# Performance work log

Hardware: AMD Instinct MI355X
Metric: run time of the kernel (lower is better)

The kernel has to match this reference:

```python
import jax, jax.numpy as jnp
import numpy as np

DIM = 256
N_SLOTS = 4096
HEADS = 4
RANK = 32
TOPK = 32
BATCH = 4
LN_EPS = 1e-5


def _layer_norm(x, gamma, beta):
    m = jnp.mean(x, axis=-1, keepdims=True)
    v = jnp.var(x, axis=-1, keepdims=True)
    return (x - m) * jax.lax.rsqrt(v + LN_EPS) * gamma + beta


def _unit_normalize(v):
    n = jnp.sqrt(jnp.sum(v * v, axis=-1, keepdims=True))
    return v / jnp.maximum(n, 1e-6)


def _signed_softmax(x, axis):
    # sign(x) * softmax(|x|): 'signed_abs_softmax' compression
    return jnp.sign(x) * jax.nn.softmax(jnp.abs(x), axis=axis)


def setup_inputs() -> dict:
    key = jax.random.key(0)
    k1, k2, k3, k4 = jax.random.split(key, 4)
    return {
        "batch_size": BATCH,
        "init_state": 0.02 * jax.random.normal(k1, (N_SLOTS,), dtype=jnp.float32),
        "init_val": 0.02 * jax.random.normal(k2, (N_SLOTS, DIM), dtype=jnp.float32),
        "ln_gamma": jnp.ones((DIM,), dtype=jnp.float32),
        "ln_beta": jnp.zeros((DIM,), dtype=jnp.float32),
        "Wq": jax.random.normal(k3, (HEADS, DIM, RANK), dtype=jnp.float32) / np.sqrt(DIM),
        "Wk": jax.random.normal(k4, (HEADS, DIM, RANK), dtype=jnp.float32) / np.sqrt(DIM),
    }


def reference(batch_size, init_state, init_val, ln_gamma, ln_beta, Wq, Wk):
    B = int(batch_size)
    # ---- initialize(): LayerNorm + unit-normalize values, signed-softmax state ----
    val0 = _unit_normalize(_layer_norm(init_val, ln_gamma, ln_beta))  # [N, D]
    val = jnp.broadcast_to(val0[None], (B, N_SLOTS, DIM))             # [B, N, D]
    state = _signed_softmax(jnp.broadcast_to(init_state[None], (B, N_SLOTS)), axis=-1)

    # ---- SparsePropagation: low-rank multi-head pairwise scores ----
    q = jnp.einsum("bnd,hdr->bhnr", val, Wq)  # [B, H, N, R]
    k = jnp.einsum("bnd,hdr->bhnr", val, Wk)  # [B, H, N, R]
    scores = jnp.einsum("bhnr,bhmr->bnm", q, k)  # [B, N, N] (summed over heads)

    # top-k edges per node by |score| (signed routing)
    _, idx = jax.lax.top_k(jnp.abs(scores), TOPK)            # idx: [B, N, K]
    s = jnp.take_along_axis(scores, idx, axis=-1)            # signed scores [B, N, K]
    w = _signed_softmax(s, axis=-1)                          # edge weights [B, N, K]

    # gather neighbor values and aggregate messages
    vj = jnp.take_along_axis(val[:, None, :, :].repeat(1, axis=1),
                             idx[..., None].repeat(DIM, axis=-1),
                             axis=2) if False else val[jnp.arange(B)[:, None, None], idx]  # [B, N, K, D]
    msg = jnp.einsum("bnk,bnkd->bnd", w, vj)                 # [B, N, D]

    # residual + direction-only (unit-normalized) values
    out_val = _unit_normalize(val + msg)
    return out_val
```

## Files before the change

### kernel.cpp

```cpp
#include <hip/hip_runtime.h>
#include <hip/hip_bf16.h>
#include <math.h>

#define N_SLOTS 4096
#define DIM 256
#define HEADS 4
#define RANK 32
#define TOPK 32
#define QK 128

typedef __attribute__((ext_vector_type(8))) short short8;
typedef __attribute__((ext_vector_type(4))) float f32x4;

__device__ __forceinline__ float block_sum256(float v, float* red) {
#pragma unroll
  for (int o = 32; o > 0; o >>= 1) v += __shfl_xor(v, o);
  int lane = threadIdx.x & 63, wid = threadIdx.x >> 6;
  if (lane == 0) red[wid] = v;
  __syncthreads();
  v = red[0] + red[1] + red[2] + red[3];
  __syncthreads();
  return v;
}

__global__ __launch_bounds__(256) void ln_unit_kernel(
    const float* __restrict__ x, const float* __restrict__ g,
    const float* __restrict__ b, float* __restrict__ val0) {
  __shared__ float red[4];
  int n = blockIdx.x, t = threadIdx.x;
  float v = x[n * DIM + t];
  float mean = block_sum256(v, red) * (1.0f / DIM);
  float d = v - mean;
  float var = block_sum256(d * d, red) * (1.0f / DIM);
  float y = d * rsqrtf(var + 1e-5f) * g[t] + b[t];
  float ss = block_sum256(y * y, red);
  y = y / fmaxf(sqrtf(ss), 1e-6f);
  val0[n * DIM + t] = y;
}

#define QR 4
__global__ __launch_bounds__(256) void qk2_kernel(
    const float* __restrict__ val0, const float* __restrict__ Wq,
    const float* __restrict__ Wk, __hip_bfloat16* __restrict__ qh,
    __hip_bfloat16* __restrict__ ql, __hip_bfloat16* __restrict__ kh,
    __hip_bfloat16* __restrict__ kl) {
  __shared__ float vrow[QR][DIM];
  int t = threadIdx.x;
  int n0 = blockIdx.x * QR;
#pragma unroll
  for (int j = 0; j < QR; ++j) {
    int idx = j * 256 + t;
    vrow[idx >> 8][idx & 255] = val0[(size_t)n0 * DIM + idx];
  }
  __syncthreads();
  int half = t >> 7, u = t & 127, h = u >> 5, r = u & 31;
  const float* wp = (half ? Wk : Wq) + (size_t)h * DIM * RANK + r;
  float acc[QR];
#pragma unroll
  for (int i = 0; i < QR; ++i) acc[i] = 0.f;
#pragma unroll 8
  for (int d = 0; d < DIM; ++d) {
    float w = wp[d * RANK];
#pragma unroll
    for (int i = 0; i < QR; ++i) acc[i] = fmaf(vrow[i][d], w, acc[i]);
  }
  __hip_bfloat16* oh = half ? kh : qh;
  __hip_bfloat16* ol = half ? kl : ql;
#pragma unroll
  for (int i = 0; i < QR; ++i) {
    size_t o = (size_t)(n0 + i) * QK + u;
    __hip_bfloat16 hi = __float2bfloat16(acc[i]);
    oh[o] = hi;
    ol[o] = __float2bfloat16(acc[i] - __bfloat162float(hi));
  }
}

#define TPAD 68
__device__ __forceinline__ int swz(int i) { return i ^ ((i >> 4) & 7); }

__global__ __launch_bounds__(256) void scores_mfma_kernel(
    const __hip_bfloat16* __restrict__ qh, const __hip_bfloat16* __restrict__ ql,
    const __hip_bfloat16* __restrict__ kh, const __hip_bfloat16* __restrict__ kl,
    float* __restrict__ S, int row0) {
  __shared__ short8 kfrag[2048];
  __shared__ float tile[64 * TPAD];
  int tid = threadIdx.x;
  int w = tid >> 6, l = tid & 63;
  int r = l & 15, g = l >> 4;
  int bcol = blockIdx.x * 64;
  int arow = row0 + blockIdx.y * 64 + w * 16 + r;

  const __hip_bfloat16* qhp = qh + (size_t)arow * QK + g * 8;
  const __hip_bfloat16* qlp = ql + (size_t)arow * QK + g * 8;
  short8 ah[4], al[4];
#pragma unroll
  for (int kc = 0; kc < 4; ++kc) {
    ah[kc] = *(const short8*)(qhp + kc * 32);
    al[kc] = *(const short8*)(qlp + kc * 32);
  }

#pragma unroll
  for (int p = 0; p < 4; ++p) {
    int ci = p * 256 + tid;
    int row = ci >> 4, j = ci & 15;
    int fi = ((j >> 2) << 8) + ((row >> 4) << 6) + ((j & 3) << 4) + (row & 15);
    const __hip_bfloat16* src = kh + (size_t)(bcol + row) * QK + j * 8;
    const __hip_bfloat16* srl = kl + (size_t)(bcol + row) * QK + j * 8;
    kfrag[swz(fi)] = *(const short8*)src;
    kfrag[swz(1024 + fi)] = *(const short8*)srl;
  }
  __syncthreads();

  f32x4 acc[4];
#pragma unroll
  for (int c = 0; c < 4; ++c) acc[c] = (f32x4){0.f, 0.f, 0.f, 0.f};
#pragma unroll
  for (int c = 0; c < 4; ++c) {
#pragma unroll
    for (int kc = 0; kc < 4; ++kc) {
      short8 bh = kfrag[swz(kc * 256 + c * 64 + l)];
      short8 bl = kfrag[swz(1024 + kc * 256 + c * 64 + l)];
      acc[c] = __builtin_amdgcn_mfma_f32_16x16x32_bf16(ah[kc], bh, acc[c], 0, 0, 0);
      acc[c] = __builtin_amdgcn_mfma_f32_16x16x32_bf16(ah[kc], bl, acc[c], 0, 0, 0);
      acc[c] = __builtin_amdgcn_mfma_f32_16x16x32_bf16(al[kc], bh, acc[c], 0, 0, 0);
    }
  }
#pragma unroll
  for (int c = 0; c < 4; ++c)
#pragma unroll
    for (int reg = 0; reg < 4; ++reg)
      tile[(w * 16 + g * 4 + reg) * TPAD + c * 16 + r] = acc[c][reg];
  __syncthreads();
  float* Stile = S + ((size_t)blockIdx.y * gridDim.x + blockIdx.x) * 4096;
#pragma unroll
  for (int p = 0; p < 4; ++p) {
    int f = p * 256 + tid;
    int row = f >> 4, f4 = f & 15;
    float4 val = *(const float4*)&tile[row * TPAD + f4 * 4];
    *(float4*)(Stile + (size_t)f * 4) = val;
  }
}

__global__ __launch_bounds__(256) void topk_agg_kernel(
    const float* __restrict__ S, const float* __restrict__ val0,
    float* __restrict__ out, int row0, int B) {
  __shared__ int hist[4 * 2048];
  __shared__ int s_wtot[4];
  __shared__ int s_piv[2];
  __shared__ int s_selidx[TOPK];
  __shared__ float s_selval[TOPK];
  __shared__ int s_tiei[64];
  __shared__ float s_tiev[64];
  __shared__ int s_cnt[2];
  __shared__ float s_w[TOPK];
  __shared__ float red[4];

  int t = threadIdx.x, lane = t & 63, wid = t >> 6;
  int n = row0 + blockIdx.x;
  int rt = blockIdx.x >> 6, rl = blockIdx.x & 63;
  const float* Sbase = S + (size_t)rt * 64 * N_SLOTS + (size_t)rl * 64;

  float v[16];
  unsigned key[16];
#pragma unroll
  for (int it = 0; it < 4; ++it) {
    int idx4 = it * 256 + t;
    int ct = idx4 >> 4, f4 = idx4 & 15;
    float4 f = *(const float4*)(Sbase + (size_t)ct * 4096 + f4 * 4);
    v[it * 4 + 0] = f.x; v[it * 4 + 1] = f.y;
    v[it * 4 + 2] = f.z; v[it * 4 + 3] = f.w;
  }
#pragma unroll
  for (int e = 0; e < 16; ++e) key[e] = __float_as_uint(fabsf(v[e]));

  unsigned prefix = 0u, pmask = 0u;
  int Kr = TOPK;
  const int SH[3] = {21, 10, 0};
  const unsigned BM[3] = {2047u, 2047u, 1023u};
#pragma unroll
  for (int rnd = 0; rnd < 3; ++rnd) {
    int shift = SH[rnd];
    unsigned bmask = BM[rnd];
#pragma unroll
    for (int cp = 0; cp < 4; ++cp) {
      *(int4*)&hist[cp * 2048 + t * 8] = (int4){0, 0, 0, 0};
      *(int4*)&hist[cp * 2048 + t * 8 + 4] = (int4){0, 0, 0, 0};
    }
    __syncthreads();
#pragma unroll
    for (int e = 0; e < 16; ++e)
      if ((key[e] & pmask) == prefix)
        atomicAdd(&hist[wid * 2048 + ((key[e] >> shift) & bmask)], 1);
    __syncthreads();
    int hl[8], sl[8];
    {
      int4 a0 = *(const int4*)&hist[0 * 2048 + t * 8];
      int4 a1 = *(const int4*)&hist[1 * 2048 + t * 8];
      int4 a2 = *(const int4*)&hist[2 * 2048 + t * 8];
      int4 a3 = *(const int4*)&hist[3 * 2048 + t * 8];
      int4 b0 = *(const int4*)&hist[0 * 2048 + t * 8 + 4];
      int4 b1 = *(const int4*)&hist[1 * 2048 + t * 8 + 4];
      int4 b2 = *(const int4*)&hist[2 * 2048 + t * 8 + 4];
      int4 b3 = *(const int4*)&hist[3 * 2048 + t * 8 + 4];
      hl[0] = a0.x + a1.x + a2.x + a3.x; hl[1] = a0.y + a1.y + a2.y + a3.y;
      hl[2] = a0.z + a1.z + a2.z + a3.z; hl[3] = a0.w + a1.w + a2.w + a3.w;
      hl[4] = b0.x + b1.x + b2.x + b3.x; hl[5] = b0.y + b1.y + b2.y + b3.y;
      hl[6] = b0.z + b1.z + b2.z + b3.z; hl[7] = b0.w + b1.w + b2.w + b3.w;
    }
    int run = 0;
#pragma unroll
    for (int j = 7; j >= 0; --j) { run += hl[j]; sl[j] = run; }
    int ws = run;
#pragma unroll
    for (int o = 1; o < 64; o <<= 1) {
      int tmp = __shfl_down(ws, o);
      if (lane + o < 64) ws += tmp;
    }
    if (lane == 0) s_wtot[wid] = ws;
    __syncthreads();
    int above = ws - run;
    for (int ww = wid + 1; ww < 4; ++ww) above += s_wtot[ww];
#pragma unroll
    for (int j = 0; j < 8; ++j) {
      int suf = sl[j] + above;
      if (suf >= Kr && suf - hl[j] < Kr) {
        s_piv[0] = t * 8 + j;
        s_piv[1] = suf - hl[j];
      }
    }
    __syncthreads();
    prefix |= ((unsigned)s_piv[0]) << shift;
    pmask |= bmask << shift;
    Kr -= s_piv[1];
    __syncthreads();
  }
  unsigned T = prefix;

  if (t < 2) s_cnt[t] = 0;
  __syncthreads();
#pragma unroll
  for (int e = 0; e < 16; ++e) {
    int idx4 = (e >> 2) * 256 + t;
    int m = (idx4 >> 4) * 64 + (idx4 & 15) * 4 + (e & 3);
    if (key[e] > T) {
      int p = atomicAdd(&s_cnt[0], 1);
      s_selidx[p] = m;
      s_selval[p] = v[e];
    } else if (key[e] == T) {
      int p = atomicAdd(&s_cnt[1], 1);
      if (p < 64) { s_tiei[p] = m; s_tiev[p] = v[e]; }
    }
  }
  __syncthreads();
  int cnt_gt = s_cnt[0];
  int need = TOPK - cnt_gt;
  if (wid == 0) {
    int ce = min(s_cnt[1], 64);
    int cand = (lane < ce) ? s_tiei[lane] : 0x7fffffff;
    float cval = (lane < ce) ? s_tiev[lane] : 0.0f;
    for (int i = 0; i < need; ++i) {
      int mi = cand;
#pragma unroll
      for (int o = 32; o > 0; o >>= 1) mi = min(mi, __shfl_xor(mi, o));
      if (cand == mi) {
        s_selidx[cnt_gt + i] = cand;
        s_selval[cnt_gt + i] = cval;
        cand = 0x7fffffff;
      }
    }
    float sv = (lane < TOPK) ? s_selval[lane] : 0.0f;
    float aa = fabsf(sv);
    float mx = aa;
#pragma unroll
    for (int o = 16; o > 0; o >>= 1) mx = fmaxf(mx, __shfl_xor(mx, o, 32));
    float e2 = expf(aa - mx);
    float sum = e2;
#pragma unroll
    for (int o = 16; o > 0; o >>= 1) sum += __shfl_xor(sum, o, 32);
    if (lane < TOPK) {
      float sgn = (sv > 0.f) ? 1.f : ((sv < 0.f) ? -1.f : 0.f);
      s_w[lane] = sgn * e2 / sum;
    }
  }
  __syncthreads();

  float base = val0[n * DIM + t];
  float msg = 0.f;
#pragma unroll
  for (int kk = 0; kk < TOPK; ++kk)
    msg = fmaf(s_w[kk], val0[(size_t)s_selidx[kk] * DIM + t], msg);
  float o = base + msg;
  float ss = block_sum256(o * o, red);
  o *= 1.0f / fmaxf(sqrtf(ss), 1e-6f);
  for (int b = 0; b < B; ++b) out[((size_t)b * N_SLOTS + n) * DIM + t] = o;
}

extern "C" void kernel_launch(void* const* d_in, const int* in_sizes, int n_in,
                              void* d_out, int out_size, void* d_ws, size_t ws_size,
                              hipStream_t stream) {
  const float* init_val = (const float*)d_in[2];
  const float* g = (const float*)d_in[3];
  const float* b = (const float*)d_in[4];
  const float* Wq = (const float*)d_in[5];
  const float* Wk = (const float*)d_in[6];
  float* out = (float*)d_out;
  int B = out_size / (N_SLOTS * DIM);

  char* ws = (char*)d_ws;
  float* val0 = (float*)ws;
  __hip_bfloat16* qh = (__hip_bfloat16*)(ws + ((size_t)4 << 20));
  __hip_bfloat16* ql = (__hip_bfloat16*)(ws + ((size_t)5 << 20));
  __hip_bfloat16* kh = (__hip_bfloat16*)(ws + ((size_t)6 << 20));
  __hip_bfloat16* kl = (__hip_bfloat16*)(ws + ((size_t)7 << 20));
  float* S = (float*)(ws + ((size_t)8 << 20));
  size_t rem = ws_size > ((size_t)8 << 20) ? ws_size - ((size_t)8 << 20) : 0;
  int rows_chunk = (int)((rem / ((size_t)N_SLOTS * sizeof(float))) / 64) * 64;
  if (rows_chunk > 1024) rows_chunk = 1024;
  if (rows_chunk < 64) rows_chunk = 64;

  hipLaunchKernelGGL(ln_unit_kernel, dim3(N_SLOTS), dim3(DIM), 0, stream,
                     init_val, g, b, val0);
  hipLaunchKernelGGL(qk2_kernel, dim3(N_SLOTS / QR), dim3(256), 0, stream,
                     val0, Wq, Wk, qh, ql, kh, kl);
  for (int start = 0; start < N_SLOTS; start += rows_chunk) {
    int rows = N_SLOTS - start;
    if (rows > rows_chunk) rows = rows_chunk;
    hipLaunchKernelGGL(scores_mfma_kernel, dim3(N_SLOTS / 64, rows / 64),
                       dim3(256), 0, stream, qh, ql, kh, kl, S, start);
    hipLaunchKernelGGL(topk_agg_kernel, dim3(rows), dim3(256), 0, stream,
                       S, val0, out, start, B);
  }
}
```

Before: 201.8 us.

## Compute two row tiles per scores block and store MFMA results directly

```diff
diff --git a/kernel.cpp b/kernel.cpp
--- a/kernel.cpp
+++ b/kernel.cpp
@@ -75,7 +75,6 @@
   }
 }
 
-#define TPAD 68
 __device__ __forceinline__ int swz(int i) { return i ^ ((i >> 4) & 7); }
 
 __global__ __launch_bounds__(256) void scores_mfma_kernel(
@@ -83,20 +82,27 @@
     const __hip_bfloat16* __restrict__ kh, const __hip_bfloat16* __restrict__ kl,
     float* __restrict__ S, int row0) {
   __shared__ short8 kfrag[2048];
-  __shared__ float tile[64 * TPAD];
   int tid = threadIdx.x;
   int w = tid >> 6, l = tid & 63;
   int r = l & 15, g = l >> 4;
   int bcol = blockIdx.x * 64;
-  int arow = row0 + blockIdx.y * 64 + w * 16 + r;
-
-  const __hip_bfloat16* qhp = qh + (size_t)arow * QK + g * 8;
-  const __hip_bfloat16* qlp = ql + (size_t)arow * QK + g * 8;
-  short8 ah[4], al[4];
-#pragma unroll
-  for (int kc = 0; kc < 4; ++kc) {
-    ah[kc] = *(const short8*)(qhp + kc * 32);
-    al[kc] = *(const short8*)(qlp + kc * 32);
+  int rowbase = row0 + blockIdx.y * 128;
+
+  short8 ah0[4], al0[4], ah1[4], al1[4];
+  {
+    int arow0 = rowbase + w * 16 + r;
+    int arow1 = arow0 + 64;
+    const __hip_bfloat16* p0h = qh + (size_t)arow0 * QK + g * 8;
+    const __hip_bfloat16* p0l = ql + (size_t)arow0 * QK + g * 8;
+    const __hip_bfloat16* p1h = qh + (size_t)arow1 * QK + g * 8;
+    const __hip_bfloat16* p1l = ql + (size_t)arow1 * QK + g * 8;
+#pragma unroll
+    for (int kc = 0; kc < 4; ++kc) {
+      ah0[kc] = *(const short8*)(p0h + kc * 32);
+      al0[kc] = *(const short8*)(p0l + kc * 32);
+      ah1[kc] = *(const short8*)(p1h + kc * 32);
+      al1[kc] = *(const short8*)(p1l + kc * 32);
+    }
   }
 
 #pragma unroll
@@ -104,41 +110,42 @@
     int ci = p * 256 + tid;
     int row = ci >> 4, j = ci & 15;
     int fi = ((j >> 2) << 8) + ((row >> 4) << 6) + ((j & 3) << 4) + (row & 15);
-    const __hip_bfloat16* src = kh + (size_t)(bcol + row) * QK + j * 8;
-    const __hip_bfloat16* srl = kl + (size_t)(bcol + row) * QK + j * 8;
-    kfrag[swz(fi)] = *(const short8*)src;
-    kfrag[swz(1024 + fi)] = *(const short8*)srl;
-  }
-  __syncthreads();
-
-  f32x4 acc[4];
-#pragma unroll
-  for (int c = 0; c < 4; ++c) acc[c] = (f32x4){0.f, 0.f, 0.f, 0.f};
+    kfrag[swz(fi)] = *(const short8*)(kh + (size_t)(bcol + row) * QK + j * 8);
+    kfrag[swz(1024 + fi)] = *(const short8*)(kl + (size_t)(bcol + row) * QK + j * 8);
+  }
+  __syncthreads();
+
+  f32x4 acc0[4], acc1[4];
+#pragma unroll
+  for (int c = 0; c < 4; ++c) {
+    acc0[c] = (f32x4){0.f, 0.f, 0.f, 0.f};
+    acc1[c] = (f32x4){0.f, 0.f, 0.f, 0.f};
+  }
 #pragma unroll
   for (int c = 0; c < 4; ++c) {
 #pragma unroll
     for (int kc = 0; kc < 4; ++kc) {
       short8 bh = kfrag[swz(kc * 256 + c * 64 + l)];
       short8 bl = kfrag[swz(1024 + kc * 256 + c * 64 + l)];
-      acc[c] = __builtin_amdgcn_mfma_f32_16x16x32_bf16(ah[kc], bh, acc[c], 0, 0, 0);
-      acc[c] = __builtin_amdgcn_mfma_f32_16x16x32_bf16(ah[kc], bl, acc[c], 0, 0, 0);
-      acc[c] = __builtin_amdgcn_mfma_f32_16x16x32_bf16(al[kc], bh, acc[c], 0, 0, 0);
-    }
-  }
+      acc0[c] = __builtin_amdgcn_mfma_f32_16x16x32_bf16(ah0[kc], bh, acc0[c], 0, 0, 0);
+      acc0[c] = __builtin_amdgcn_mfma_f32_16x16x32_bf16(ah0[kc], bl, acc0[c], 0, 0, 0);
+      acc0[c] = __builtin_amdgcn_mfma_f32_16x16x32_bf16(al0[kc], bh, acc0[c], 0, 0, 0);
+      acc1[c] = __builtin_amdgcn_mfma_f32_16x16x32_bf16(ah1[kc], bh, acc1[c], 0, 0, 0);
+      acc1[c] = __builtin_amdgcn_mfma_f32_16x16x32_bf16(ah1[kc], bl, acc1[c], 0, 0, 0);
+      acc1[c] = __builtin_amdgcn_mfma_f32_16x16x32_bf16(al1[kc], bh, acc1[c], 0, 0, 0);
+    }
+  }
+  int ry0 = blockIdx.y * 2;
+  int trow = w * 16 + g * 4;
+  float* St0 = S + ((size_t)ry0 * 64 + blockIdx.x) * 4096;
+  float* St1 = S + ((size_t)(ry0 + 1) * 64 + blockIdx.x) * 4096;
 #pragma unroll
   for (int c = 0; c < 4; ++c)
 #pragma unroll
-    for (int reg = 0; reg < 4; ++reg)
-      tile[(w * 16 + g * 4 + reg) * TPAD + c * 16 + r] = acc[c][reg];
-  __syncthreads();
-  float* Stile = S + ((size_t)blockIdx.y * gridDim.x + blockIdx.x) * 4096;
-#pragma unroll
-  for (int p = 0; p < 4; ++p) {
-    int f = p * 256 + tid;
-    int row = f >> 4, f4 = f & 15;
-    float4 val = *(const float4*)&tile[row * TPAD + f4 * 4];
-    *(float4*)(Stile + (size_t)f * 4) = val;
-  }
+    for (int reg = 0; reg < 4; ++reg) {
+      St0[(trow + reg) * 64 + c * 16 + r] = acc0[c][reg];
+      St1[(trow + reg) * 64 + c * 16 + r] = acc1[c][reg];
+    }
 }
 
 __global__ __launch_bounds__(256) void topk_agg_kernel(
@@ -314,9 +321,9 @@
   __hip_bfloat16* kl = (__hip_bfloat16*)(ws + ((size_t)7 << 20));
   float* S = (float*)(ws + ((size_t)8 << 20));
   size_t rem = ws_size > ((size_t)8 << 20) ? ws_size - ((size_t)8 << 20) : 0;
-  int rows_chunk = (int)((rem / ((size_t)N_SLOTS * sizeof(float))) / 64) * 64;
-  if (rows_chunk > 1024) rows_chunk = 1024;
-  if (rows_chunk < 64) rows_chunk = 64;
+  int rows_chunk = (int)((rem / ((size_t)N_SLOTS * sizeof(float))) / 128) * 128;
+  if (rows_chunk > N_SLOTS) rows_chunk = N_SLOTS;
+  if (rows_chunk < 128) rows_chunk = 128;
 
   hipLaunchKernelGGL(ln_unit_kernel, dim3(N_SLOTS), dim3(DIM), 0, stream,
                      init_val, g, b, val0);
@@ -325,7 +332,7 @@
   for (int start = 0; start < N_SLOTS; start += rows_chunk) {
     int rows = N_SLOTS - start;
     if (rows > rows_chunk) rows = rows_chunk;
-    hipLaunchKernelGGL(scores_mfma_kernel, dim3(N_SLOTS / 64, rows / 64),
+    hipLaunchKernelGGL(scores_mfma_kernel, dim3(N_SLOTS / 64, rows / 128),
                        dim3(256), 0, stream, qh, ql, kh, kl, S, start);
     hipLaunchKernelGGL(topk_agg_kernel, dim3(rows), dim3(256), 0, stream,
                        S, val0, out, start, B);
```

After: 169.6 us. 15.9% less time.
